# Kernel tuning notes

Measured on AMD Instinct MI355X. Metric: run time of the kernel, lower is better.

The kernel has to match this reference:

```python
import jax, jax.numpy as jnp
import numpy as np

EMBED = 512
HEADS = 8
HEAD_DIM = EMBED // HEADS
MLP_HIDDEN = EMBED * 4
EPS = 1e-5


def _layernorm(x, g, b):
    mu = jnp.mean(x, axis=-1, keepdims=True)
    var = jnp.var(x, axis=-1, keepdims=True)
    return (x - mu) * jax.lax.rsqrt(var + EPS) * g + b


def setup_inputs() -> dict:
    key = jax.random.key(0)
    ks = jax.random.split(key, 12)
    s = 0.02
    return {
        "x": jax.random.normal(ks[0], (4, 2048, EMBED), dtype=jnp.float32),
        "ln1_g": jnp.ones((EMBED,), jnp.float32),
        "ln1_b": jnp.zeros((EMBED,), jnp.float32),
        "w_qkv": jax.random.normal(ks[1], (EMBED, 3 * EMBED), jnp.float32) * s,
        "b_qkv": jnp.zeros((3 * EMBED,), jnp.float32),
        "w_proj": jax.random.normal(ks[2], (EMBED, EMBED), jnp.float32) * s,
        "b_proj": jnp.zeros((EMBED,), jnp.float32),
        "ln2_g": jnp.ones((EMBED,), jnp.float32),
        "ln2_b": jnp.zeros((EMBED,), jnp.float32),
        "w1": jax.random.normal(ks[3], (EMBED, MLP_HIDDEN), jnp.float32) * s,
        "b1": jnp.zeros((MLP_HIDDEN,), jnp.float32),
        "w2": jax.random.normal(ks[4], (MLP_HIDDEN, EMBED), jnp.float32) * s,
        "b2": jnp.zeros((EMBED,), jnp.float32),
    }


def reference(x, ln1_g, ln1_b, w_qkv, b_qkv, w_proj, b_proj, ln2_g, ln2_b, w1, b1, w2, b2):
    B, N, C = x.shape
    scale = HEAD_DIM ** -0.5
    h = _layernorm(x, ln1_g, ln1_b)
    qkv = h @ w_qkv + b_qkv                       # [B,N,3C]
    qkv = qkv.reshape(B, N, 3, HEADS, HEAD_DIM)
    q = qkv[:, :, 0].transpose(0, 2, 1, 3)        # [B,H,N,D]
    k = qkv[:, :, 1].transpose(0, 2, 1, 3)
    v = qkv[:, :, 2].transpose(0, 2, 1, 3)
    attn = jnp.einsum('bhnd,bhmd->bhnm', q, k) * scale
    attn = jax.nn.softmax(attn, axis=-1)
    h = jnp.einsum('bhnm,bhmd->bhnd', attn, v)    # [B,H,N,D]
    h = h.transpose(0, 2, 1, 3).reshape(B, N, C)
    h = h @ w_proj + b_proj
    x = x + h
    m = _layernorm(x, ln2_g, ln2_b)
    m = jax.nn.gelu(m @ w1 + b1, approximate=False) @ w2 + b2
    return x + m
```

## Files before the change

kernel.cpp:

```cpp
#include <hip/hip_runtime.h>
#include <hip/hip_bf16.h>

typedef unsigned short u16;
typedef unsigned int u32;
typedef __attribute__((ext_vector_type(8))) __bf16 bf16x8;
typedef __attribute__((ext_vector_type(4))) float f32x4;
typedef __attribute__((ext_vector_type(16))) float f32x16;

#define LOG2E 1.4426950408889634f

__device__ __forceinline__ u16 f2bf(float f) {
  union { __hip_bfloat16 h; u16 u; } cv;
  cv.h = __float2bfloat16(f);
  return cv.u;
}

__device__ __forceinline__ float bf2f(u16 u) {
  union { u32 u; float f; } cv;
  cv.u = ((u32)u) << 16;
  return cv.f;
}

__device__ __forceinline__ u32 pk2(float a, float b) {
  return (u32)f2bf(a) | ((u32)f2bf(b) << 16);
}

#define EXP2 __builtin_amdgcn_exp2f

__device__ __forceinline__ f32x4 mfma16(bf16x8 a, bf16x8 b, f32x4 c) {
  return __builtin_amdgcn_mfma_f32_16x16x32_bf16(a, b, c, 0, 0, 0);
}
__device__ __forceinline__ f32x16 mfma32(bf16x8 a, bf16x8 b, f32x16 c) {
  return __builtin_amdgcn_mfma_f32_32x32x16_bf16(a, b, c, 0, 0, 0);
}

__device__ __forceinline__ void gload16(const u16* g, u16* lds) {
  __builtin_amdgcn_global_load_lds(
      (const __attribute__((address_space(1))) u32*)g,
      (__attribute__((address_space(3))) u32*)lds, 16, 0, 0);
}

__global__ __launch_bounds__(256) void prep_kernel(
    const float* __restrict__ w_qkv, u16* __restrict__ wqkvT,
    const float* __restrict__ w_proj, u16* __restrict__ wprojT,
    const float* __restrict__ w1, u16* __restrict__ w1T,
    const float* __restrict__ w2, u16* __restrict__ w2T,
    const float* __restrict__ X, const float* __restrict__ gam,
    const float* __restrict__ bet, u16* __restrict__ Y) {
  __shared__ float T[64][65];
  const int bid = blockIdx.x;
  if (bid < 768) {
    const float* W; u16* WT; int K, N, base;
    if (bid < 192)      { W = w_qkv; WT = wqkvT; K = 512;  N = 1536; base = 0; }
    else if (bid < 256) { W = w_proj; WT = wprojT; K = 512; N = 512; base = 192; }
    else if (bid < 512) { W = w1;   WT = w1T;   K = 512;  N = 2048; base = 256; }
    else                { W = w2;   WT = w2T;   K = 2048; N = 512;  base = 512; }
    int b = bid - base;
    int ntx = N >> 6;
    int bx = b % ntx, by = b / ntx;
    int tx = threadIdx.x & 63, ty = threadIdx.x >> 6;
#pragma unroll
    for (int i = 0; i < 64; i += 4)
      T[ty + i][tx] = W[(size_t)(by * 64 + ty + i) * N + bx * 64 + tx];
    __syncthreads();
#pragma unroll
    for (int i = 0; i < 64; i += 4)
      WT[(size_t)(bx * 64 + ty + i) * K + by * 64 + tx] = f2bf(T[tx][ty + i]);
  } else {
    int wid = threadIdx.x >> 6, l = threadIdx.x & 63;
    int row = (bid - 768) * 4 + wid;
    const float4* xp = reinterpret_cast<const float4*>(X + (size_t)row * 512);
    float4 a = xp[l], c = xp[l + 64];
    float s  = a.x + a.y + a.z + a.w + c.x + c.y + c.z + c.w;
    float s2 = a.x*a.x + a.y*a.y + a.z*a.z + a.w*a.w
             + c.x*c.x + c.y*c.y + c.z*c.z + c.w*c.w;
#pragma unroll
    for (int m = 1; m < 64; m <<= 1) { s += __shfl_xor(s, m); s2 += __shfl_xor(s2, m); }
    float mu = s * (1.f / 512.f);
    float rs = rsqrtf(s2 * (1.f / 512.f) - mu * mu + 1e-5f);
    const float4* gp = reinterpret_cast<const float4*>(gam);
    const float4* bp = reinterpret_cast<const float4*>(bet);
    float4 g0 = gp[l], g1 = gp[l + 64], b0 = bp[l], b1 = bp[l + 64];
    ushort4 o;
    o.x = f2bf((a.x - mu) * rs * g0.x + b0.x);
    o.y = f2bf((a.y - mu) * rs * g0.y + b0.y);
    o.z = f2bf((a.z - mu) * rs * g0.z + b0.z);
    o.w = f2bf((a.w - mu) * rs * g0.w + b0.w);
    reinterpret_cast<ushort4*>(Y + (size_t)row * 512)[l] = o;
    o.x = f2bf((c.x - mu) * rs * g1.x + b1.x);
    o.y = f2bf((c.y - mu) * rs * g1.y + b1.y);
    o.z = f2bf((c.z - mu) * rs * g1.z + b1.z);
    o.w = f2bf((c.w - mu) * rs * g1.w + b1.w);
    reinterpret_cast<ushort4*>(Y + (size_t)row * 512)[l + 64] = o;
  }
}

__global__ __launch_bounds__(256) void ln4_kernel(const float* __restrict__ X,
                                                  const float* __restrict__ gam,
                                                  const float* __restrict__ bet,
                                                  u16* __restrict__ Y) {
  int wid = threadIdx.x >> 6, l = threadIdx.x & 63;
  int row = blockIdx.x * 4 + wid;
  const float4* xp = reinterpret_cast<const float4*>(X + (size_t)row * 512);
  float4 a = xp[l], c = xp[l + 64];
  float s  = a.x + a.y + a.z + a.w + c.x + c.y + c.z + c.w;
  float s2 = a.x*a.x + a.y*a.y + a.z*a.z + a.w*a.w
           + c.x*c.x + c.y*c.y + c.z*c.z + c.w*c.w;
#pragma unroll
  for (int m = 1; m < 64; m <<= 1) { s += __shfl_xor(s, m); s2 += __shfl_xor(s2, m); }
  float mu = s * (1.f / 512.f);
  float rs = rsqrtf(s2 * (1.f / 512.f) - mu * mu + 1e-5f);
  const float4* gp = reinterpret_cast<const float4*>(gam);
  const float4* bp = reinterpret_cast<const float4*>(bet);
  float4 g0 = gp[l], g1 = gp[l + 64], b0 = bp[l], b1 = bp[l + 64];
  ushort4 o;
  o.x = f2bf((a.x - mu) * rs * g0.x + b0.x);
  o.y = f2bf((a.y - mu) * rs * g0.y + b0.y);
  o.z = f2bf((a.z - mu) * rs * g0.z + b0.z);
  o.w = f2bf((a.w - mu) * rs * g0.w + b0.w);
  reinterpret_cast<ushort4*>(Y + (size_t)row * 512)[l] = o;
  o.x = f2bf((c.x - mu) * rs * g1.x + b1.x);
  o.y = f2bf((c.y - mu) * rs * g1.y + b1.y);
  o.z = f2bf((c.z - mu) * rs * g1.z + b1.z);
  o.w = f2bf((c.w - mu) * rs * g1.w + b1.w);
  reinterpret_cast<ushort4*>(Y + (size_t)row * 512)[l + 64] = o;
}

template <int EPI>
__global__ __launch_bounds__(512)
__attribute__((amdgpu_waves_per_eu(4)))
void gemm_bt(const u16* __restrict__ A, const u16* __restrict__ BT,
             int M, int N, int K,
             const float* __restrict__ bias,
             u16* __restrict__ outU,
             u16* __restrict__ Qo, u16* __restrict__ Ko, u16* __restrict__ VTo) {
  constexpr int BM = 128, BN = 128, WC = 4, FM = 4;
  __shared__ u16 As[2][BM * 32];
  __shared__ u16 Bs[2][BN * 32];
  const int tid = threadIdx.x;
  const int wid = tid >> 6, l = tid & 63;
  const int lg = l >> 4, ll = l & 15;
  const int nx = gridDim.x;
  const int id = blockIdx.y * nx + blockIdx.x;
  const int cpx = (nx * gridDim.y) >> 3;
  const int wg = (id & 7) * cpx + (id >> 3);
  const int m0 = (wg / nx) * BM, n0 = (wg % nx) * BN;
  const int wm = (wid / WC) * (BM / 2), wn = (wid % WC) * 32;
  const f32x4 zf = {0.f, 0.f, 0.f, 0.f};
  f32x4 acc[FM][2];
#pragma unroll
  for (int i = 0; i < FM; i++) { acc[i][0] = zf; acc[i][1] = zf; }

  const int grow = tid >> 2;
  const int gcol = (tid & 3) ^ ((grow >> 1) & 3);
  const u16* Asrc = A + (size_t)(m0 + grow) * K + gcol * 8;
  const u16* Bsrc = BT + (size_t)(n0 + grow) * K + gcol * 8;

  const int r0a = wm + ll;
  const int aoff0 = (r0a * 4 + (lg ^ ((r0a >> 1) & 3))) * 8;
  const int r0b = wn + ll;
  const int boff0 = (r0b * 4 + (lg ^ ((r0b >> 1) & 3))) * 8;

  const int nt = K >> 5;
  gload16(Asrc, &As[0][tid * 8]);
  gload16(Bsrc, &Bs[0][tid * 8]);
  for (int t = 0; t < nt; t++) {
    __syncthreads();
    if (t + 1 < nt) {
      gload16(Asrc + ((t + 1) << 5), &As[(t + 1) & 1][tid * 8]);
      gload16(Bsrc + ((t + 1) << 5), &Bs[(t + 1) & 1][tid * 8]);
    }
    const u16* A_ = As[t & 1];
    const u16* B_ = Bs[t & 1];
    bf16x8 af[FM], bfr[2];
#pragma unroll
    for (int i = 0; i < FM; i++)
      af[i] = *reinterpret_cast<const bf16x8*>(A_ + aoff0 + 512 * i);
    bfr[0] = *reinterpret_cast<const bf16x8*>(B_ + boff0);
    bfr[1] = *reinterpret_cast<const bf16x8*>(B_ + boff0 + 512);
#pragma unroll
    for (int i = 0; i < FM; i++) {
      acc[i][0] = mfma16(af[i], bfr[0], acc[i][0]);
      acc[i][1] = mfma16(af[i], bfr[1], acc[i][1]);
    }
  }

#pragma unroll
  for (int i = 0; i < FM; i++) {
#pragma unroll
    for (int j = 0; j < 2; j++) {
      int col = n0 + wn + j * 16 + ll;
      float bcol2 = bias[col];
      int rbase = m0 + wm + i * 16 + lg * 4;
#pragma unroll
      for (int r = 0; r < 4; r++) {
        int row = rbase + r;
        float val = acc[i][j][r] + bcol2;
        if (EPI == 0) {
          int bi = row >> 11, nseq = row & 2047;
          int t = col >> 9, rem = col & 511;
          int hh = rem >> 6, dd = rem & 63;
          size_t hidx = ((size_t)((bi << 3) + hh) * 2048 + nseq) * 64 + dd;
          if (t == 0)      Qo[hidx] = f2bf(val * (0.125f * LOG2E));
          else if (t == 1) Ko[hidx] = f2bf(val);
          else VTo[((size_t)((bi << 3) + hh) * 64 + dd) * 2048 + nseq] = f2bf(val);
        } else {
          float y = 0.7978845608f * (val + 0.044715f * val * val * val);
          float e = EXP2(2.0f * LOG2E * y);
          float t2 = 1.0f - 2.0f / (e + 1.0f);
          outU[(size_t)row * 2048 + col] = f2bf(0.5f * val * (1.0f + t2));
        }
      }
    }
  }
}

__global__ __launch_bounds__(256)
__attribute__((amdgpu_waves_per_eu(4)))
void gemm_bt64(const u16* __restrict__ A, const u16* __restrict__ BT,
               int M, int N, int K,
               const float* __restrict__ bias,
               const float* __restrict__ resid,
               float* __restrict__ outF) {
  __shared__ u16 As[2][64 * 64];
  __shared__ u16 Bs[2][64 * 64];
  const int tid = threadIdx.x;
  const int wid = tid >> 6, l = tid & 63;
  const int lg = l >> 4, ll = l & 15;
  const int nx = gridDim.x;
  const int id = blockIdx.y * nx + blockIdx.x;
  const int cpx = (nx * gridDim.y) >> 3;
  const int wg = (id & 7) * cpx + (id >> 3);
  const int m0 = (wg / nx) * 64, n0 = (wg % nx) * 64;
  const int wm = (wid >> 1) * 32, wn = (wid & 1) * 32;
  const f32x4 zf = {0.f, 0.f, 0.f, 0.f};
  f32x4 acc[2][2];
  acc[0][0] = zf; acc[0][1] = zf; acc[1][0] = zf; acc[1][1] = zf;

  int srow[2], scol[2];
#pragma unroll
  for (int j = 0; j < 2; j++) {
    int p = j * 256 + tid;
    srow[j] = p >> 3;
    scol[j] = (p & 7) ^ (srow[j] & 7);
  }

  const int ra = wm + ll;
  const int aoff0 = ra * 64 + (lg ^ (ra & 7)) * 8;
  const int rb = wn + ll;
  const int boff0 = rb * 64 + (lg ^ (rb & 7)) * 8;

  auto stage = [&](int kt, int buf) {
#pragma unroll
    for (int j = 0; j < 2; j++) {
      int p = j * 256 + tid;
      gload16(A + (size_t)(m0 + srow[j]) * K + kt + scol[j] * 8, &As[buf][p * 8]);
      gload16(BT + (size_t)(n0 + srow[j]) * K + kt + scol[j] * 8, &Bs[buf][p * 8]);
    }
  };

  const int nt = K >> 6;
  stage(0, 0);
  for (int t = 0; t < nt; t++) {
    __syncthreads();
    if (t + 1 < nt) stage((t + 1) << 6, (t + 1) & 1);
    const u16* A_ = As[t & 1];
    const u16* B_ = Bs[t & 1];
#pragma unroll
    for (int kk = 0; kk < 2; kk++) {
      const int ax = kk ? (aoff0 ^ 32) : aoff0;
      const int bx = kk ? (boff0 ^ 32) : boff0;
      bf16x8 a0 = *reinterpret_cast<const bf16x8*>(A_ + ax);
      bf16x8 a1 = *reinterpret_cast<const bf16x8*>(A_ + ax + 1024);
      bf16x8 b0 = *reinterpret_cast<const bf16x8*>(B_ + bx);
      bf16x8 b1 = *reinterpret_cast<const bf16x8*>(B_ + bx + 1024);
      acc[0][0] = mfma16(a0, b0, acc[0][0]);
      acc[0][1] = mfma16(a0, b1, acc[0][1]);
      acc[1][0] = mfma16(a1, b0, acc[1][0]);
      acc[1][1] = mfma16(a1, b1, acc[1][1]);
    }
  }

#pragma unroll
  for (int i = 0; i < 2; i++) {
#pragma unroll
    for (int j = 0; j < 2; j++) {
      int col = n0 + wn + j * 16 + ll;
      float bcol2 = bias[col];
      int rbase = m0 + wm + i * 16 + lg * 4;
#pragma unroll
      for (int r = 0; r < 4; r++) {
        size_t idx = (size_t)(rbase + r) * 512 + col;
        outF[idx] = acc[i][j][r] + bcol2 + resid[idx];
      }
    }
  }
}

__global__ __launch_bounds__(256)
__attribute__((amdgpu_waves_per_eu(4)))
void attn_kernel(const u16* __restrict__ Q,
                 const u16* __restrict__ Kt,
                 const u16* __restrict__ VT,
                 u16* __restrict__ Opart,
                 float* __restrict__ Stat) {
  __shared__ __align__(16) u16 Kbuf[2][64 * 64];
  __shared__ __align__(16) u16 Vbuf[2][64 * 64];
  const int tid = threadIdx.x;
  const int wid = tid >> 6, l = tid & 63;
  const int lq = l & 31, h = l >> 5;
  const int b = blockIdx.z, hd = blockIdx.y;
  const int qt = blockIdx.x >> 2, sp = blockIdx.x & 3;
  const int qbase = qt * 128 + wid * 32;
  const int kv0 = sp * 512;
  const size_t hoff = (size_t)(b * 8 + hd) * 2048 * 64;
  const u16* Qh = Q + hoff;
  const u16* Kh = Kt + hoff;
  const u16* Vh = VT + hoff;

  bf16x8 qf[4];
#pragma unroll
  for (int s = 0; s < 4; s++)
    qf[s] = *reinterpret_cast<const bf16x8*>(Qh + (size_t)(qbase + lq) * 64 + s * 16 + h * 8);

  int koff[4];
#pragma unroll
  for (int s = 0; s < 4; s++)
    koff[s] = (lq * 8 + ((s * 2 + h) ^ (lq & 7))) * 8;

  f32x16 oacc[2];
#pragma unroll
  for (int r = 0; r < 16; r++) { oacc[0][r] = 0.f; oacc[1][r] = 0.f; }
  float ps0 = 0.f, ps1 = 0.f;

  auto stage = [&](int kb, int buf) {
#pragma unroll
    for (int half = 0; half < 2; half++) {
      int g0 = half * 256 + wid * 64;
      int p = g0 + l;
      int row = p >> 3;
      int c = (p & 7) ^ (row & 7);
      gload16(Kh + (size_t)(kb + row) * 64 + c * 8, &Kbuf[buf][g0 * 8]);
      gload16(Vh + (size_t)row * 2048 + kb + c * 8, &Vbuf[buf][g0 * 8]);
    }
  };

  stage(kv0, 0);
  for (int i = 0; i < 8; i++) {
    __syncthreads();
    if (i < 7) stage(kv0 + (i + 1) * 64, (i + 1) & 1);
    const u16* Kc = Kbuf[i & 1];
    const u16* Vc = Vbuf[i & 1];

#pragma unroll
    for (int t = 0; t < 2; t++) {
      f32x16 st;
#pragma unroll
      for (int r = 0; r < 16; r++) st[r] = 0.f;
      __builtin_amdgcn_s_setprio(1);
      if (t == 0) {
#pragma unroll
        for (int s = 0; s < 4; s++)
          st = mfma32(*reinterpret_cast<const bf16x8*>(Kc + koff[s]), qf[s], st);
      } else {
#pragma unroll
        for (int s = 0; s < 4; s++)
          st = mfma32(*reinterpret_cast<const bf16x8*>(Kc + koff[s] + 2048), qf[s], st);
      }
      __builtin_amdgcn_s_setprio(0);

#pragma unroll
      for (int j = 0; j < 16; j += 4) {
        float p0 = EXP2(st[j + 0]);
        float p1 = EXP2(st[j + 1]);
        float p2 = EXP2(st[j + 2]);
        float p3 = EXP2(st[j + 3]);
        st[j + 0] = p0; st[j + 1] = p1; st[j + 2] = p2; st[j + 3] = p3;
        ps0 += p0 + p2; ps1 += p1 + p3;
      }

      u32 w0 = pk2(st[0], st[1]),   w1 = pk2(st[2], st[3]);
      u32 w2 = pk2(st[4], st[5]),   w3 = pk2(st[6], st[7]);
      u32 w4 = pk2(st[8], st[9]),   w5 = pk2(st[10], st[11]);
      u32 w6 = pk2(st[12], st[13]), w7 = pk2(st[14], st[15]);
      uint4 pa0, pa1;
#if __has_builtin(__builtin_amdgcn_permlane32_swap)
      auto r02 = __builtin_amdgcn_permlane32_swap(w0, w2, false, false);
      auto r13 = __builtin_amdgcn_permlane32_swap(w1, w3, false, false);
      auto r46 = __builtin_amdgcn_permlane32_swap(w4, w6, false, false);
      auto r57 = __builtin_amdgcn_permlane32_swap(w5, w7, false, false);
      pa0.x = (u32)r02[0]; pa0.y = (u32)r13[0]; pa0.z = (u32)r02[1]; pa0.w = (u32)r13[1];
      pa1.x = (u32)r46[0]; pa1.y = (u32)r57[0]; pa1.z = (u32)r46[1]; pa1.w = (u32)r57[1];
#else
      u32 ra2, rb2;
      ra2 = (u32)__shfl_xor((int)(h ? w0 : w2), 32);
      rb2 = (u32)__shfl_xor((int)(h ? w1 : w3), 32);
      pa0.x = h ? ra2 : w0; pa0.y = h ? rb2 : w1;
      pa0.z = h ? w0 : ra2; pa0.w = h ? w1 : rb2;
      ra2 = (u32)__shfl_xor((int)(h ? w4 : w6), 32);
      rb2 = (u32)__shfl_xor((int)(h ? w5 : w7), 32);
      pa1.x = h ? ra2 : w4; pa1.y = h ? rb2 : w5;
      pa1.z = h ? w4 : ra2; pa1.w = h ? w5 : rb2;
#endif
      union { uint4 u; bf16x8 v; } p0u, p1u;
      p0u.u = pa0; p1u.u = pa1;
      __builtin_amdgcn_s_setprio(1);
      if (t == 0) {
        oacc[0] = mfma32(p0u.v, *reinterpret_cast<const bf16x8*>(Vc + koff[0]), oacc[0]);
        oacc[0] = mfma32(p1u.v, *reinterpret_cast<const bf16x8*>(Vc + koff[1]), oacc[0]);
        oacc[1] = mfma32(p0u.v, *reinterpret_cast<const bf16x8*>(Vc + koff[0] + 2048), oacc[1]);
        oacc[1] = mfma32(p1u.v, *reinterpret_cast<const bf16x8*>(Vc + koff[1] + 2048), oacc[1]);
      } else {
        oacc[0] = mfma32(p0u.v, *reinterpret_cast<const bf16x8*>(Vc + koff[2]), oacc[0]);
        oacc[0] = mfma32(p1u.v, *reinterpret_cast<const bf16x8*>(Vc + koff[3]), oacc[0]);
        oacc[1] = mfma32(p0u.v, *reinterpret_cast<const bf16x8*>(Vc + koff[2] + 2048), oacc[1]);
        oacc[1] = mfma32(p1u.v, *reinterpret_cast<const bf16x8*>(Vc + koff[3] + 2048), oacc[1]);
      }
      __builtin_amdgcn_s_setprio(0);
    }
  }

  float lsum = ps0 + ps1;
  lsum += __shfl_xor(lsum, 32);

  u16* Op = Opart + (size_t)sp * 8192 * 512;
#pragma unroll
  for (int r = 0; r < 16; r++) {
    const int qr = (r & 3) + 8 * (r >> 2) + 4 * h;
    size_t row = (size_t)b * 2048 + qbase + qr;
#pragma unroll
    for (int dt = 0; dt < 2; dt++) {
      int col = hd * 64 + dt * 32 + lq;
      Op[row * 512 + col] = f2bf(oacc[dt][r]);
    }
  }
  if (h == 0)
    Stat[(size_t)sp * 32 * 2048 + (size_t)(b * 8 + hd) * 2048 + qbase + lq] = lsum;
}

__global__ __launch_bounds__(256) void attn_merge(const u16* __restrict__ Opart,
                                                  const float* __restrict__ Stat,
                                                  u16* __restrict__ O) {
  int gid = blockIdx.x * 256 + threadIdx.x;
  int row = gid >> 6;
  int c8 = (gid & 63) * 8;
  int hd = c8 >> 6;
  int bh = (row >> 11) * 8 + hd;
  int n = row & 2047;
  float L = 0.f;
  float acc[8];
#pragma unroll
  for (int j = 0; j < 8; j++) acc[j] = 0.f;
#pragma unroll
  for (int p = 0; p < 4; p++) {
    L += Stat[(size_t)p * 32 * 2048 + (size_t)bh * 2048 + n];
    const ushort4* pp = reinterpret_cast<const ushort4*>(
        Opart + (size_t)p * 8192 * 512 + (size_t)row * 512 + c8);
    ushort4 v0 = pp[0], v1 = pp[1];
    acc[0] += bf2f(v0.x); acc[1] += bf2f(v0.y);
    acc[2] += bf2f(v0.z); acc[3] += bf2f(v0.w);
    acc[4] += bf2f(v1.x); acc[5] += bf2f(v1.y);
    acc[6] += bf2f(v1.z); acc[7] += bf2f(v1.w);
  }
  float li = 1.0f / L;
  ushort4 o0, o1;
  o0.x = f2bf(acc[0] * li); o0.y = f2bf(acc[1] * li);
  o0.z = f2bf(acc[2] * li); o0.w = f2bf(acc[3] * li);
  o1.x = f2bf(acc[4] * li); o1.y = f2bf(acc[5] * li);
  o1.z = f2bf(acc[6] * li); o1.w = f2bf(acc[7] * li);
  ushort4* op = reinterpret_cast<ushort4*>(O + (size_t)row * 512 + c8);
  op[0] = o0;
  op[1] = o1;
}

extern "C" void kernel_launch(void* const* d_in, const int* in_sizes, int n_in,
                              void* d_out, int out_size, void* d_ws, size_t ws_size,
                              hipStream_t stream) {
  const float* x      = (const float*)d_in[0];
  const float* ln1_g  = (const float*)d_in[1];
  const float* ln1_b  = (const float*)d_in[2];
  const float* w_qkv  = (const float*)d_in[3];
  const float* b_qkv  = (const float*)d_in[4];
  const float* w_proj = (const float*)d_in[5];
  const float* b_proj = (const float*)d_in[6];
  const float* ln2_g  = (const float*)d_in[7];
  const float* ln2_b  = (const float*)d_in[8];
  const float* w1     = (const float*)d_in[9];
  const float* b1     = (const float*)d_in[10];
  const float* w2     = (const float*)d_in[11];
  const float* b2     = (const float*)d_in[12];
  float* out = (float*)d_out;

  const int M = 8192;
  char* w = (char*)d_ws;
  u16* wqkvT  = (u16*)w; w += (size_t)1536 * 512 * 2;
  u16* wprojT = (u16*)w; w += (size_t)512 * 512 * 2;
  u16* w1T    = (u16*)w; w += (size_t)2048 * 512 * 2;
  u16* w2T    = (u16*)w; w += (size_t)512 * 2048 * 2;
  u16* h1     = (u16*)w; w += (size_t)M * 512 * 2;
  u16* Qb     = (u16*)w; w += (size_t)M * 512 * 2;
  u16* Kb     = (u16*)w; w += (size_t)M * 512 * 2;
  u16* VTb    = (u16*)w; w += (size_t)M * 512 * 2;
  u16* attn   = (u16*)w; w += (size_t)M * 512 * 2;
  u16* h2     = (u16*)w; w += (size_t)M * 512 * 2;
  u16* mid    = (u16*)w; w += (size_t)M * 2048 * 2;
  float* Stat = (float*)w; w += (size_t)4 * 32 * 2048 * sizeof(float);
  u16* Opart = (u16*)mid;

  prep_kernel<<<2816, 256, 0, stream>>>(w_qkv, wqkvT, w_proj, wprojT,
                                        w1, w1T, w2, w2T,
                                        x, ln1_g, ln1_b, h1);

  gemm_bt<0><<<dim3(1536 / 128, M / 128), 512, 0, stream>>>(
      h1, wqkvT, M, 1536, 512, b_qkv, nullptr, Qb, Kb, VTb);

  attn_kernel<<<dim3(64, 8, 4), 256, 0, stream>>>(Qb, Kb, VTb, Opart, Stat);
  attn_merge<<<M * 64 / 256, 256, 0, stream>>>(Opart, Stat, attn);

  gemm_bt64<<<dim3(512 / 64, M / 64), 256, 0, stream>>>(
      attn, wprojT, M, 512, 512, b_proj, x, out);

  ln4_kernel<<<M / 4, 256, 0, stream>>>(out, ln2_g, ln2_b, h2);

  gemm_bt<2><<<dim3(2048 / 128, M / 128), 512, 0, stream>>>(
      h2, w1T, M, 2048, 512, b1, mid, nullptr, nullptr, nullptr);

  gemm_bt64<<<dim3(512 / 64, M / 64), 256, 0, stream>>>(
      mid, w2T, M, 512, 2048, b2, out, out);
}
```

Baseline: 169.9 us.

## Deepen GEMM K-tile to 64 with 8-way swizzle and vectorize V-transpose stores

The bf16 GEMM kernel now stages 64-wide K slices instead of 32 per double-buffered step, with a new XOR swizzle over 8 chunks and two MFMA sub-steps per barrier. This halves the number of __syncthreads and global-load rounds per tile, at the cost of doubling shared memory per block, which may limit occupancy. The QKV epilogue also writes the transposed V output as one 4-element vector store instead of four scalar strided stores, and hoists the index math for Q and K.

Result: faster. 165.1 us (-2.8%).

```diff
diff --git a/kernel.cpp b/kernel.cpp
--- a/kernel.cpp
+++ b/kernel.cpp
@@ -135,8 +135,8 @@
              u16* __restrict__ outU,
              u16* __restrict__ Qo, u16* __restrict__ Ko, u16* __restrict__ VTo) {
   constexpr int BM = 128, BN = 128, WC = 4, FM = 4;
-  __shared__ u16 As[2][BM * 32];
-  __shared__ u16 Bs[2][BN * 32];
+  __shared__ u16 As[2][BM * 64];
+  __shared__ u16 Bs[2][BN * 64];
   const int tid = threadIdx.x;
   const int wid = tid >> 6, l = tid & 63;
   const int lg = l >> 4, ll = l & 15;
@@ -151,37 +151,50 @@
 #pragma unroll
   for (int i = 0; i < FM; i++) { acc[i][0] = zf; acc[i][1] = zf; }
 
-  const int grow = tid >> 2;
-  const int gcol = (tid & 3) ^ ((grow >> 1) & 3);
-  const u16* Asrc = A + (size_t)(m0 + grow) * K + gcol * 8;
-  const u16* Bsrc = BT + (size_t)(n0 + grow) * K + gcol * 8;
+  int srow[2], scol[2];
+#pragma unroll
+  for (int j = 0; j < 2; j++) {
+    int p = j * 512 + tid;
+    srow[j] = p >> 3;
+    scol[j] = (p & 7) ^ (srow[j] & 7);
+  }
 
   const int r0a = wm + ll;
-  const int aoff0 = (r0a * 4 + (lg ^ ((r0a >> 1) & 3))) * 8;
+  const int aoff0 = r0a * 64 + (lg ^ (r0a & 7)) * 8;
   const int r0b = wn + ll;
-  const int boff0 = (r0b * 4 + (lg ^ ((r0b >> 1) & 3))) * 8;
-
-  const int nt = K >> 5;
-  gload16(Asrc, &As[0][tid * 8]);
-  gload16(Bsrc, &Bs[0][tid * 8]);
+  const int boff0 = r0b * 64 + (lg ^ (r0b & 7)) * 8;
+
+  auto stage = [&](int kt, int buf) {
+#pragma unroll
+    for (int j = 0; j < 2; j++) {
+      int p = j * 512 + tid;
+      gload16(A + (size_t)(m0 + srow[j]) * K + kt + scol[j] * 8, &As[buf][p * 8]);
+      gload16(BT + (size_t)(n0 + srow[j]) * K + kt + scol[j] * 8, &Bs[buf][p * 8]);
+    }
+  };
+
+  const int nt = K >> 6;
+  stage(0, 0);
   for (int t = 0; t < nt; t++) {
     __syncthreads();
-    if (t + 1 < nt) {
-      gload16(Asrc + ((t + 1) << 5), &As[(t + 1) & 1][tid * 8]);
-      gload16(Bsrc + ((t + 1) << 5), &Bs[(t + 1) & 1][tid * 8]);
-    }
+    if (t + 1 < nt) stage((t + 1) << 6, (t + 1) & 1);
     const u16* A_ = As[t & 1];
     const u16* B_ = Bs[t & 1];
-    bf16x8 af[FM], bfr[2];
-#pragma unroll
-    for (int i = 0; i < FM; i++)
-      af[i] = *reinterpret_cast<const bf16x8*>(A_ + aoff0 + 512 * i);
-    bfr[0] = *reinterpret_cast<const bf16x8*>(B_ + boff0);
-    bfr[1] = *reinterpret_cast<const bf16x8*>(B_ + boff0 + 512);
-#pragma unroll
-    for (int i = 0; i < FM; i++) {
-      acc[i][0] = mfma16(af[i], bfr[0], acc[i][0]);
-      acc[i][1] = mfma16(af[i], bfr[1], acc[i][1]);
+#pragma unroll
+    for (int kk = 0; kk < 2; kk++) {
+      const int ax = kk ? (aoff0 ^ 32) : aoff0;
+      const int bx = kk ? (boff0 ^ 32) : boff0;
+      bf16x8 af[FM], bfr[2];
+#pragma unroll
+      for (int i = 0; i < FM; i++)
+        af[i] = *reinterpret_cast<const bf16x8*>(A_ + ax + 1024 * i);
+      bfr[0] = *reinterpret_cast<const bf16x8*>(B_ + bx);
+      bfr[1] = *reinterpret_cast<const bf16x8*>(B_ + bx + 1024);
+#pragma unroll
+      for (int i = 0; i < FM; i++) {
+        acc[i][0] = mfma16(af[i], bfr[0], acc[i][0]);
+        acc[i][1] = mfma16(af[i], bfr[1], acc[i][1]);
+      }
     }
   }
 
@@ -192,23 +205,35 @@
       int col = n0 + wn + j * 16 + ll;
       float bcol2 = bias[col];
       int rbase = m0 + wm + i * 16 + lg * 4;
-#pragma unroll
-      for (int r = 0; r < 4; r++) {
-        int row = rbase + r;
-        float val = acc[i][j][r] + bcol2;
-        if (EPI == 0) {
-          int bi = row >> 11, nseq = row & 2047;
-          int t = col >> 9, rem = col & 511;
-          int hh = rem >> 6, dd = rem & 63;
-          size_t hidx = ((size_t)((bi << 3) + hh) * 2048 + nseq) * 64 + dd;
-          if (t == 0)      Qo[hidx] = f2bf(val * (0.125f * LOG2E));
-          else if (t == 1) Ko[hidx] = f2bf(val);
-          else VTo[((size_t)((bi << 3) + hh) * 64 + dd) * 2048 + nseq] = f2bf(val);
+      if (EPI == 0) {
+        int bi = rbase >> 11, nseq0 = rbase & 2047;
+        int t = col >> 9, rem = col & 511;
+        int hh = rem >> 6, dd = rem & 63;
+        if (t == 2) {
+          ushort4 v;
+          v.x = f2bf(acc[i][j][0] + bcol2);
+          v.y = f2bf(acc[i][j][1] + bcol2);
+          v.z = f2bf(acc[i][j][2] + bcol2);
+          v.w = f2bf(acc[i][j][3] + bcol2);
+          *reinterpret_cast<ushort4*>(
+              VTo + ((size_t)((bi << 3) + hh) * 64 + dd) * 2048 + nseq0) = v;
         } else {
+          size_t hidx = ((size_t)((bi << 3) + hh) * 2048 + nseq0) * 64 + dd;
+#pragma unroll
+          for (int r = 0; r < 4; r++) {
+            float val = acc[i][j][r] + bcol2;
+            if (t == 0) Qo[hidx + (size_t)r * 64] = f2bf(val * (0.125f * LOG2E));
+            else        Ko[hidx + (size_t)r * 64] = f2bf(val);
+          }
+        }
+      } else {
+#pragma unroll
+        for (int r = 0; r < 4; r++) {
+          float val = acc[i][j][r] + bcol2;
           float y = 0.7978845608f * (val + 0.044715f * val * val * val);
           float e = EXP2(2.0f * LOG2E * y);
           float t2 = 1.0f - 2.0f / (e + 1.0f);
-          outU[(size_t)row * 2048 + col] = f2bf(0.5f * val * (1.0f + t2));
+          outU[(size_t)(rbase + r) * 2048 + col] = f2bf(0.5f * val * (1.0f + t2));
         }
       }
     }
```
